# Optimization experiments

Hardware: AMD Instinct MI355X
Metric: run time of the kernel (lower is better)

## Reference

```python
import jax, jax.numpy as jnp
import numpy as np

IN_FEATURES = 4096
NF = 16384  # output channels (GPT-2 Conv1d 'nf')
B, S = 8, 32


def setup_inputs() -> dict:
    key = jax.random.key(0)
    kx, kw, ks, kb = jax.random.split(key, 4)
    x = jax.random.normal(kx, (B, S, IN_FEATURES), dtype=jnp.float32)
    # int8 quantized weight in [-128, 127]
    weight = jax.random.randint(kw, (IN_FEATURES, NF), -128, 128, dtype=jnp.int32).astype(jnp.int8)
    # per-output-channel dequant scale (small positive values, as |w0|max/128)
    scale = (jax.random.uniform(ks, (1, NF), dtype=jnp.float32) * 0.02 + 1e-4)
    bias = jax.random.normal(kb, (NF,), dtype=jnp.float32)
    return {"x": x, "weight": weight, "scale": scale, "bias": bias}


def reference(x, weight, scale, bias):
    # size_out = x.shape[:-1] + (nf,)
    size_out = x.shape[:-1] + (bias.shape[0],)
    x2 = x.reshape(-1, x.shape[-1])                      # [T, in]
    y = jnp.matmul(x2, weight.astype(x.dtype))            # dequant-to-fp then GEMM: [T, nf]
    y = y * scale + bias                                  # per-channel scale, bias add
    return y.reshape(size_out)
```

## Files before the change

kernel.cpp:

```cpp
#include <hip/hip_runtime.h>
#include <stdint.h>


typedef short bf16x8 __attribute__((ext_vector_type(8)));
typedef float f32x16 __attribute__((ext_vector_type(16)));
typedef int   i32x4  __attribute__((ext_vector_type(4)));
typedef int   i32x2  __attribute__((ext_vector_type(2)));
typedef unsigned short u16x4 __attribute__((ext_vector_type(4)));

#define K_DIM 4096
#define N_DIM 16384
#define BK 128
#define BN 64
#define NIT (K_DIM / BK)
#define KSTEPS 256

__device__ __forceinline__ unsigned fbits(float f) {
  union { float f; unsigned u; } c; c.f = f; return c.u;
}
__device__ __forceinline__ unsigned short bf16rne(float f) {
  unsigned u = fbits(f);
  return (unsigned short)((u + 0x7FFFu + ((u >> 16) & 1u)) >> 16);
}

__global__ __launch_bounds__(256) void cvt_x_frag(const float* __restrict__ x,
                                                  unsigned short* __restrict__ xb) {
  int c    = blockIdx.x * 256 + threadIdx.x;
  int lane = c & 63;
  int ks   = (c >> 6) & 255;
  int mt   = c >> 14;
  int row  = mt * 32 + (lane & 31);
  int k0   = ks * 16 + (lane >> 5) * 8;
  const float4* p = (const float4*)(x + row * K_DIM + k0);
  float4 v0 = p[0], v1 = p[1];
  u16x4 o0, o1;
  o0.x = bf16rne(v0.x); o0.y = bf16rne(v0.y); o0.z = bf16rne(v0.z); o0.w = bf16rne(v0.w);
  o1.x = bf16rne(v1.x); o1.y = bf16rne(v1.y); o1.z = bf16rne(v1.z); o1.w = bf16rne(v1.w);
  u16x4* dst = (u16x4*)(xb + (size_t)c * 8);
  dst[0] = o0;
  dst[1] = o1;
}

__global__ __launch_bounds__(512, 2) void gemm_qconv(
    const unsigned short* __restrict__ xb,
    const int* __restrict__ w,
    const float* __restrict__ scale,
    const float* __restrict__ bias,
    float* __restrict__ out) {
  __shared__ i32x4 Blds[16 * 64];

  const int tid  = threadIdx.x;
  const int lane = tid & 63;
  const int wave = tid >> 6;
  const int l31  = lane & 31;
  const int half = lane >> 5;
  const int wm   = wave >> 1;
  const int wn   = wave & 1;
  const int n0   = blockIdx.x * BN;

  const int n2 = tid & 31;
  const int k8 = tid >> 5;
  const int sW = k8 >> 1;
  const int hW = k8 & 1;
  const int nnA = n2 * 2, nnB = n2 * 2 + 1;
  const int slotA = ((nnA >> 5) * 8 + sW) * 64 + (hW * 32 + (nnA & 31));
  const int slotB = ((nnB >> 5) * 8 + sW) * 64 + (hW * 32 + (nnB & 31));

  const int* wbase = w + (k8 * 8) * N_DIM + n0 + n2 * 2;

  i32x2 L[8];
#pragma unroll
  for (int i = 0; i < 8; ++i) L[i] = *(const i32x2*)(wbase + i * N_DIM);

  f32x16 acc0 = {};
  f32x16 acc1 = {};

  const bf16x8* afrag0 = (const bf16x8*)(xb + (size_t)((wm * 2 + 0) * KSTEPS) * 64 * 8);
  const bf16x8* afrag1 = (const bf16x8*)(xb + (size_t)((wm * 2 + 1) * KSTEPS) * 64 * 8);

#pragma unroll 1
  for (int it = 0; it < NIT; ++it) {
    i32x4 chA, chB;
#pragma unroll
    for (int d = 0; d < 4; ++d) {
      float a0 = (float)L[2 * d].x,     a1 = (float)L[2 * d + 1].x;
      float b0 = (float)L[2 * d].y,     b1 = (float)L[2 * d + 1].y;
      chA[d] = (int)__builtin_amdgcn_perm(fbits(a1), fbits(a0), 0x07060302u);
      chB[d] = (int)__builtin_amdgcn_perm(fbits(b1), fbits(b0), 0x07060302u);
    }
    Blds[slotA] = chA;
    Blds[slotB] = chB;
    __syncthreads();

    bf16x8 A0[8], A1[8];
#pragma unroll
    for (int s = 0; s < 8; ++s) {
      A0[s] = afrag0[(it * 8 + s) * 64 + lane];
      A1[s] = afrag1[(it * 8 + s) * 64 + lane];
    }

    if (it + 1 < NIT) {
      const int* wp = wbase + (it + 1) * BK * N_DIM;
#pragma unroll
      for (int i = 0; i < 8; ++i) L[i] = *(const i32x2*)(wp + i * N_DIM);
    }

#pragma unroll
    for (int s = 0; s < 8; ++s) {
      bf16x8 b = *(const bf16x8*)&Blds[(wn * 8 + s) * 64 + lane];
      acc0 = __builtin_amdgcn_mfma_f32_32x32x16_bf16(A0[s], b, acc0, 0, 0, 0);
      acc1 = __builtin_amdgcn_mfma_f32_32x32x16_bf16(A1[s], b, acc1, 0, 0, 0);
    }
    __syncthreads();
  }

  const int n = n0 + wn * 32 + l31;
  const float sc = scale[n];
  const float bs = bias[n];
#pragma unroll
  for (int r = 0; r < 2; ++r) {
    const f32x16 acc = r ? acc1 : acc0;
#pragma unroll
    for (int g = 0; g < 16; ++g) {
      const int m = wm * 64 + r * 32 + (g & 3) + 8 * (g >> 2) + 4 * half;
      out[m * N_DIM + n] = acc[g] * sc + bs;
    }
  }
}

extern "C" void kernel_launch(void* const* d_in, const int* in_sizes, int n_in,
                              void* d_out, int out_size, void* d_ws, size_t ws_size,
                              hipStream_t stream) {
  const float* x     = (const float*)d_in[0];
  const int*   wgt   = (const int*)d_in[1];
  const float* scale = (const float*)d_in[2];
  const float* bias  = (const float*)d_in[3];
  float* out = (float*)d_out;
  unsigned short* xb = (unsigned short*)d_ws;

  cvt_x_frag<<<512, 256, 0, stream>>>(x, xb);
  gemm_qconv<<<256, 512, 0, stream>>>(xb, wgt, scale, bias, out);
}
```

Measured before the change: 401.7 us.

## Halve N tile, one 32-row M slice per wave, double-buffer LDS

The N tile shrinks from 64 to 32 columns, so twice as many workgroups launch, and launch bounds now allow four blocks per CU. Each wave now owns its own 32-row M slice with a single accumulator, where before it split across M and N. The B staging buffer in LDS is double-buffered, which removes the trailing barrier in each K iteration. The aim is more parallelism and less sync cost; the trade-off is that every block rereads all of the bf16 activation fragments, doubling that read traffic, and the weight loads become narrower scalar loads.

Result: no change. 402.5 us (+0.2%).

```diff
diff --git a/kernel.cpp b/kernel.cpp
--- a/kernel.cpp
+++ b/kernel.cpp
@@ -5,13 +5,12 @@
 typedef short bf16x8 __attribute__((ext_vector_type(8)));
 typedef float f32x16 __attribute__((ext_vector_type(16)));
 typedef int   i32x4  __attribute__((ext_vector_type(4)));
-typedef int   i32x2  __attribute__((ext_vector_type(2)));
 typedef unsigned short u16x4 __attribute__((ext_vector_type(4)));
 
 #define K_DIM 4096
 #define N_DIM 16384
 #define BK 128
-#define BN 64
+#define BN 32
 #define NIT (K_DIM / BK)
 #define KSTEPS 256
 
@@ -41,90 +40,73 @@
   dst[1] = o1;
 }
 
-__global__ __launch_bounds__(512, 2) void gemm_qconv(
+__global__ __launch_bounds__(512, 4) void gemm_qconv(
     const unsigned short* __restrict__ xb,
     const int* __restrict__ w,
     const float* __restrict__ scale,
     const float* __restrict__ bias,
     float* __restrict__ out) {
-  __shared__ i32x4 Blds[16 * 64];
+  __shared__ i32x4 Blds[2][8 * 64];
 
   const int tid  = threadIdx.x;
   const int lane = tid & 63;
   const int wave = tid >> 6;
   const int l31  = lane & 31;
   const int half = lane >> 5;
-  const int wm   = wave >> 1;
-  const int wn   = wave & 1;
   const int n0   = blockIdx.x * BN;
 
-  const int n2 = tid & 31;
-  const int k8 = tid >> 5;
-  const int sW = k8 >> 1;
-  const int hW = k8 & 1;
-  const int nnA = n2 * 2, nnB = n2 * 2 + 1;
-  const int slotA = ((nnA >> 5) * 8 + sW) * 64 + (hW * 32 + (nnA & 31));
-  const int slotB = ((nnB >> 5) * 8 + sW) * 64 + (hW * 32 + (nnB & 31));
+  const int kcol = tid & 31;
+  const int k8   = tid >> 5;
+  const int sW   = k8 >> 1;
+  const int hW   = k8 & 1;
+  const int slot = sW * 64 + hW * 32 + kcol;
 
-  const int* wbase = w + (k8 * 8) * N_DIM + n0 + n2 * 2;
+  const int* wbase = w + (k8 * 8) * N_DIM + n0 + kcol;
 
-  i32x2 L[8];
+  int L[8];
 #pragma unroll
-  for (int i = 0; i < 8; ++i) L[i] = *(const i32x2*)(wbase + i * N_DIM);
+  for (int i = 0; i < 8; ++i) L[i] = wbase[i * N_DIM];
 
-  f32x16 acc0 = {};
-  f32x16 acc1 = {};
+  f32x16 acc = {};
 
-  const bf16x8* afrag0 = (const bf16x8*)(xb + (size_t)((wm * 2 + 0) * KSTEPS) * 64 * 8);
-  const bf16x8* afrag1 = (const bf16x8*)(xb + (size_t)((wm * 2 + 1) * KSTEPS) * 64 * 8);
+  const bf16x8* afrag = (const bf16x8*)xb + (size_t)(wave * KSTEPS) * 64;
 
 #pragma unroll 1
   for (int it = 0; it < NIT; ++it) {
-    i32x4 chA, chB;
+    i32x4 ch;
 #pragma unroll
     for (int d = 0; d < 4; ++d) {
-      float a0 = (float)L[2 * d].x,     a1 = (float)L[2 * d + 1].x;
-      float b0 = (float)L[2 * d].y,     b1 = (float)L[2 * d + 1].y;
-      chA[d] = (int)__builtin_amdgcn_perm(fbits(a1), fbits(a0), 0x07060302u);
-      chB[d] = (int)__builtin_amdgcn_perm(fbits(b1), fbits(b0), 0x07060302u);
+      float a0 = (float)L[2 * d];
+      float a1 = (float)L[2 * d + 1];
+      ch[d] = (int)__builtin_amdgcn_perm(fbits(a1), fbits(a0), 0x07060302u);
     }
-    Blds[slotA] = chA;
-    Blds[slotB] = chB;
+    Blds[it & 1][slot] = ch;
     __syncthreads();
-
-    bf16x8 A0[8], A1[8];
-#pragma unroll
-    for (int s = 0; s < 8; ++s) {
-      A0[s] = afrag0[(it * 8 + s) * 64 + lane];
-      A1[s] = afrag1[(it * 8 + s) * 64 + lane];
-    }
 
     if (it + 1 < NIT) {
       const int* wp = wbase + (it + 1) * BK * N_DIM;
 #pragma unroll
-      for (int i = 0; i < 8; ++i) L[i] = *(const i32x2*)(wp + i * N_DIM);
+      for (int i = 0; i < 8; ++i) L[i] = wp[i * N_DIM];
     }
+
+    bf16x8 A[8];
+#pragma unroll
+    for (int s = 0; s < 8; ++s) A[s] = afrag[(it * 8 + s) * 64 + lane];
 
 #pragma unroll
     for (int s = 0; s < 8; ++s) {
-      bf16x8 b = *(const bf16x8*)&Blds[(wn * 8 + s) * 64 + lane];
-      acc0 = __builtin_amdgcn_mfma_f32_32x32x16_bf16(A0[s], b, acc0, 0, 0, 0);
-      acc1 = __builtin_amdgcn_mfma_f32_32x32x16_bf16(A1[s], b, acc1, 0, 0, 0);
+      bf16x8 b = *(const bf16x8*)&Blds[it & 1][s * 64 + lane];
+      acc = __builtin_amdgcn_mfma_f32_32x32x16_bf16(A[s], b, acc, 0, 0, 0);
     }
-    __syncthreads();
   }
 
-  const int n = n0 + wn * 32 + l31;
+  const int n = n0 + l31;
   const float sc = scale[n];
   const float bs = bias[n];
 #pragma unroll
-  for (int r = 0; r < 2; ++r) {
-    const f32x16 acc = r ? acc1 : acc0;
-#pragma unroll
-    for (int g = 0; g < 16; ++g) {
-      const int m = wm * 64 + r * 32 + (g & 3) + 8 * (g >> 2) + 4 * half;
-      out[m * N_DIM + n] = acc[g] * sc + bs;
-    }
+  for (int g = 0; g < 16; ++g) {
+    const int m = wave * 32 + (g & 3) + 8 * (g >> 2) + 4 * half;
+    out[m * N_DIM + n] = acc[g] * sc + bs;
   }
 }
 
@@ -139,5 +121,5 @@
   unsigned short* xb = (unsigned short*)d_ws;
 
   cvt_x_frag<<<512, 256, 0, stream>>>(x, xb);
-  gemm_qconv<<<256, 512, 0, stream>>>(xb, wgt, scale, bias, out);
+  gemm_qconv<<<N_DIM / BN, 512, 0, stream>>>(xb, wgt, scale, bias, out);
 }
```
